# Kernel optimization log

Hardware: AMD Instinct MI355X
Metric: run time of the kernel (lower is better)

The kernel has to match this reference:

```python
import jax, jax.numpy as jnp
import numpy as np

S = 3000    # number of candidate spans (rows of g_i)
P = 80000   # total (mention, antecedent) pairs
GI = 768    # gi_dim
DD = 20     # distance/genre/speaker embedding dim
HID = 150   # mlp hidden dim (fixed in source)
ORDER = 2   # N: one higher-order refinement pass


def setup_inputs() -> dict:
    key = jax.random.key(0)
    ks = jax.random.split(key, 18)
    gij = 3 * GI + 3 * DD
    g_i = jax.random.normal(ks[0], (S, GI), jnp.float32)
    mention_scores = jax.random.normal(ks[1], (S, 1), jnp.float32)
    # sorted segment ids: ragged antecedent counts per mention, grouped contiguously
    mention_ids = jnp.sort(jax.random.randint(ks[2], (P,), 0, S, dtype=jnp.int32))
    antecedent_ids = jax.random.randint(ks[3], (P,), 0, S, dtype=jnp.int32)
    dist_bins = jax.random.randint(ks[4], (P,), 0, 10, dtype=jnp.int32)
    genre_ids = jax.random.randint(ks[5], (P,), 0, 7, dtype=jnp.int32) + 1   # 1..7, 0 is padding_idx
    speaker_ids = jax.random.randint(ks[6], (P,), 0, 2, dtype=jnp.int32) + 1  # 1..2, 0 is padding_idx
    w = lambda k, shp: 0.02 * jax.random.normal(k, shp, jnp.float32)
    dist_emb = w(ks[7], (10, DD))
    genre_emb = w(ks[8], (8, DD)).at[0].set(0.0)     # padding_idx=0
    speaker_emb = w(ks[9], (3, DD)).at[0].set(0.0)   # padding_idx=0
    W1 = w(ks[10], (gij, HID)); b1 = jnp.zeros((HID,), jnp.float32)
    W2 = w(ks[11], (HID, HID)); b2 = jnp.zeros((HID,), jnp.float32)
    W3 = w(ks[12], (HID, 1)); b3 = jnp.zeros((1,), jnp.float32)
    Wf = w(ks[13], (2 * GI, 1)); bf = jnp.zeros((1,), jnp.float32)
    return {"g_i": g_i, "mention_scores": mention_scores, "mention_ids": mention_ids,
            "antecedent_ids": antecedent_ids, "dist_bins": dist_bins, "genre_ids": genre_ids,
            "speaker_ids": speaker_ids, "dist_emb": dist_emb, "genre_emb": genre_emb,
            "speaker_emb": speaker_emb, "W1": W1, "b1": b1, "W2": W2, "b2": b2,
            "W3": W3, "b3": b3, "Wf": Wf, "bf": bf}


def _mlp(x, W1, b1, W2, b2, W3, b3):
    h = jax.nn.relu(x @ W1 + b1)
    h = jax.nn.relu(h @ W2 + b2)
    return h @ W3 + b3


def reference(g_i, mention_scores, mention_ids, antecedent_ids, dist_bins, genre_ids,
              speaker_ids, dist_emb, genre_emb, speaker_emb, W1, b1, W2, b2, W3, b3, Wf, bf):
    phi = jnp.concatenate([dist_emb[dist_bins], genre_emb[genre_ids], speaker_emb[speaker_ids]], axis=1)  # [P,60]
    seg = dict(num_segments=S, indices_are_sorted=True)
    g = g_i
    scores = None
    for n in range(ORDER):
        i_g = g[mention_ids]                # [P,GI] gather
        j_g = g[antecedent_ids]             # [P,GI] gather
        pairs = jnp.concatenate([i_g, j_g, i_g * j_g, phi], axis=1)  # [P,gij]
        scores = _mlp(pairs, W1, b1, W2, b2, W3, b3)                 # [P,1]
        if n < ORDER - 1:
            # higher_order_refinement: ragged segment softmax + weighted scatter update
            s = scores[:, 0]
            seg_max = jax.ops.segment_max(s, mention_ids, **seg)
            safe_max = jnp.where(jnp.isfinite(seg_max), seg_max, 0.0)
            e = jnp.exp(s - safe_max[mention_ids])
            denom = jax.ops.segment_sum(e, mention_ids, **seg)
            attn = e / jnp.where(denom > 0, denom, 1.0)[mention_ids]
            weighted = jax.ops.segment_sum(attn[:, None] * j_g, mention_ids, **seg)  # [S,GI]
            counts = jax.ops.segment_sum(jnp.ones_like(s), mention_ids, **seg)
            f = jax.nn.sigmoid(jnp.concatenate([g, weighted], axis=1) @ Wf + bf)  # [S,1]
            # NOTE: faithful to the source bug: f * mention_id (the integer index), not f * mention_g
            ids_f = jnp.arange(S, dtype=g.dtype)[:, None]
            g_new = f * ids_f + (1.0 - f) * weighted
            g = jnp.where(counts[:, None] > 0, g_new, g)
    s_i = mention_scores[mention_ids]
    s_j = mention_scores[antecedent_ids]
    coref_scores = s_i + s_j + scores       # [P,1]
    # segment softmax with an extra epsilon (score 0) logit per mention
    c = coref_scores[:, 0]
    seg_max = jax.ops.segment_max(c, mention_ids, **seg)
    m = jnp.maximum(jnp.where(jnp.isfinite(seg_max), seg_max, 0.0), 0.0)  # include epsilon logit 0
    e = jnp.exp(c - m[mention_ids])
    denom = jax.ops.segment_sum(e, mention_ids, **seg) + jnp.exp(-m)
    pair_probs = e / denom[mention_ids]     # [P]
    eps_probs = jnp.exp(-m) / denom         # [S]
    return coref_scores, pair_probs, eps_probs
```

## Files before the change

### kernel.cpp

```cpp
#include <hip/hip_runtime.h>

#define GI   768
#define HID  150
#define HPAD 160
#define DDIM 20

typedef __attribute__((ext_vector_type(8))) short v8s;
typedef __attribute__((ext_vector_type(4))) float f32x4;
typedef __attribute__((ext_vector_type(16))) float f32x16;

#define MFMA(A, B, C)   __builtin_amdgcn_mfma_f32_32x32x16_bf16(A, B, C, 0, 0, 0)
#define MFMA16(A, B, C) __builtin_amdgcn_mfma_f32_16x16x32_bf16(A, B, C, 0, 0, 0)

__device__ __forceinline__ ushort bf16rn(float x) {
  unsigned u = __float_as_uint(x);
  return (ushort)((u + 0x7fffu + ((u >> 16) & 1u)) >> 16);
}
__device__ __forceinline__ void bsplit(float x, ushort& h, ushort& l) {
  h = bf16rn(x);
  float fh = __uint_as_float((unsigned)h << 16);
  l = bf16rn(x - fh);
}
__device__ __forceinline__ void tsplit(float x, ushort& h, ushort& l) {
  unsigned u = __float_as_uint(x);
  h = (ushort)(u >> 16);
  float d = x - __uint_as_float(u & 0xffff0000u);
  l = (ushort)(__float_as_uint(d) >> 16);
}
__device__ __forceinline__ uint4 pack8(const ushort* v) {
  uint4 r;
  r.x = v[0] | ((unsigned)v[1] << 16); r.y = v[2] | ((unsigned)v[3] << 16);
  r.z = v[4] | ((unsigned)v[5] << 16); r.w = v[6] | ((unsigned)v[7] << 16);
  return r;
}
__device__ __forceinline__ v8s mk8(const ushort* v) {
  union { uint4 u; v8s s; } t;
  t.u = pack8(v);
  return t.s;
}

__device__ __forceinline__ void stage16(const ushort* gsrc, ushort* ldst) {
  __builtin_amdgcn_global_load_lds(
      (const __attribute__((address_space(1))) unsigned int*)(const void*)gsrc,
      (__attribute__((address_space(3))) unsigned int*)(void*)ldst, 16, 0, 0);
}

__global__ void seg_kernel(const int* __restrict__ mI, int* __restrict__ segs,
                           int P, int S) {
  int m = blockIdx.x * 256 + threadIdx.x;
  if (m > S) return;
  int lo = 0, hi = P;
  while (lo < hi) { int mid = (lo + hi) >> 1; if (mI[mid] < m) lo = mid + 1; else hi = mid; }
  segs[m] = lo;
}

__global__ void phi_kernel(const float* __restrict__ de, const float* __restrict__ ge,
                           const float* __restrict__ se, const float* __restrict__ W1,
                           float* __restrict__ phiW) {
  int idx = blockIdx.x * 256 + threadIdx.x;
  if (idx >= 21 * HPAD) return;
  int row = idx / HPAD, h = idx % HPAD;
  float v = 0.f;
  if (h < HID) {
    const float* emb; int off;
    if (row < 10)      { emb = de + row * DDIM;        off = 0; }
    else if (row < 18) { emb = ge + (row - 10) * DDIM; off = DDIM; }
    else               { emb = se + (row - 18) * DDIM; off = 2 * DDIM; }
    for (int k = 0; k < DDIM; ++k) v += emb[k] * W1[(3 * GI + off + k) * HID + h];
  }
  phiW[row * HPAD + h] = v;
}

#define NWS  (48 * 10 * 512)
#define NW16 (20 * 24 * 512)
#define NW2B (5 * 10 * 512)
__global__ void pad2_kernel(const float* __restrict__ W1, const float* __restrict__ W2,
                            const float* __restrict__ b1, const float* __restrict__ b2,
                            const float* __restrict__ W3,
                            ushort* __restrict__ WS,
                            ushort* __restrict__ W16hi, ushort* __restrict__ W16lo,
                            ushort* __restrict__ W2Bhi, ushort* __restrict__ W2Blo,
                            float* __restrict__ b1p, float2* __restrict__ b2w3) {
  int idx = blockIdx.x * 256 + threadIdx.x;
  if (idx < NWS) {
    int s = idx / (10 * 512); int r1 = idx % (10 * 512);
    int fi = r1 / 512; int r2 = r1 % 512;
    int l = r2 / 8, j = r2 % 8;
    int c = fi >> 1, hl = fi & 1;
    int h = c * 32 + (l & 31);
    int k = s * 16 + 8 * (l >> 5) + j;
    float x = (h < HID) ? W1[(size_t)(2 * GI + k) * HID + h] : 0.f;
    ushort hh, ll; bsplit(x, hh, ll);
    WS[idx] = hl ? ll : hh; return;
  }
  idx -= NWS;
  if (idx < NW16) {
    int ct = idx / (24 * 512); int r1 = idx % (24 * 512);
    int s = r1 / 512; int r2 = r1 % 512;
    int l = r2 / 8, j = r2 % 8;
    int col = ct * 16 + (l & 15);
    int k = s * 32 + 8 * (l >> 4) + j;
    int seg = col / HPAD, h = col % HPAD;
    float x = (h < HID) ? W1[(size_t)(seg * GI + k) * HID + h] : 0.f;
    ushort hh, ll; bsplit(x, hh, ll);
    W16hi[idx] = hh; W16lo[idx] = ll; return;
  }
  idx -= NW16;
  if (idx < NW2B) {
    int rt = idx / (10 * 512); int r1 = idx % (10 * 512);
    int s = r1 / 512; int r2 = r1 % 512;
    int l = r2 / 8, j = r2 % 8;
    int h2 = rt * 32 + (l & 31);
    int k = s * 16 + 8 * (l >> 5) + j;
    float x = (k < HID && h2 < HID) ? W2[(size_t)k * HID + h2] : 0.f;
    ushort hh, ll; bsplit(x, hh, ll);
    W2Bhi[idx] = hh; W2Blo[idx] = ll; return;
  }
  idx -= NW2B;
  if (idx < HPAD) { b1p[idx] = (idx < HID) ? b1[idx] : 0.f; return; }
  idx -= HPAD;
  if (idx < HPAD) {
    b2w3[idx] = make_float2((idx < HID) ? b2[idx] : 0.f, (idx < HID) ? W3[idx] : 0.f);
    return;
  }
}

__global__ __launch_bounds__(64, 4) void pre3_kernel(
    const float* __restrict__ g, const ushort* __restrict__ W16hi,
    const ushort* __restrict__ W16lo, float* __restrict__ pre, int S) {
  const int lane = threadIdx.x;
  const int ct = blockIdx.x;
  const int row0 = blockIdx.y * 16;
  int srow = row0 + (lane & 15); if (srow >= S) srow = S - 1;
  const float* gp = g + (size_t)srow * GI + 8 * (lane >> 4);
  const ushort* wph = W16hi + ((size_t)ct * 24 * 64 + lane) * 8;
  const ushort* wpl = W16lo + ((size_t)ct * 24 * 64 + lane) * 8;

  f32x4 acc = {};
#pragma unroll 2
  for (int s = 0; s < 24; ++s) {
    const float4 a0 = *(const float4*)(gp + s * 32);
    const float4 a1 = *(const float4*)(gp + s * 32 + 4);
    const v8s bh = *(const v8s*)(wph + (size_t)s * 512);
    const v8s bl = *(const v8s*)(wpl + (size_t)s * 512);
    float xr[8] = {a0.x, a0.y, a0.z, a0.w, a1.x, a1.y, a1.z, a1.w};
    ushort hs[8], ls[8];
#pragma unroll
    for (int j = 0; j < 8; ++j) tsplit(xr[j], hs[j], ls[j]);
    const v8s ah = mk8(hs), al = mk8(ls);
    acc = MFMA16(ah, bh, acc);
    acc = MFMA16(al, bh, acc);
    acc = MFMA16(ah, bl, acc);
  }
  const int col = ct * 16 + (lane & 15);
#pragma unroll
  for (int r = 0; r < 4; ++r) {
    int sr = row0 + (lane >> 4) * 4 + r;
    if (sr < S) pre[(size_t)sr * 320 + col] = acc[r];
  }
}

__global__ __launch_bounds__(256, 3) void h1b_kernel(
    const float* __restrict__ g, const float* __restrict__ pre,
    const float* __restrict__ phiW, const ushort* __restrict__ WS,
    const float* __restrict__ b1p,
    const int* __restrict__ mI, const int* __restrict__ aI,
    const int* __restrict__ db, const int* __restrict__ ge, const int* __restrict__ sp,
    ushort* __restrict__ h1hi, ushort* __restrict__ h1lo, int P) {
  __shared__ ushort wbuf[2][10 * 512];

  const int t = threadIdx.x;
  const int lane = t & 63, wv = t >> 6;
  const int lcol = lane & 31, half = lane >> 5;

  const int nwg = gridDim.x;
  const int orig = blockIdx.x;
  const int xcd = orig & 7, idx8 = orig >> 3;
  const int qq = nwg >> 3, rq = nwg & 7;
  const int wg = (xcd < rq ? xcd * (qq + 1) : rq * (qq + 1) + (xcd - rq) * qq) + idx8;
  const int p0w = wg * 128 + wv * 32;

  const int myp = p0w + lcol;
  const int iA = mI[myp], jA = aI[myp];
  const int rdL = db[myp], rgL = 10 + ge[myp], rsL = 18 + sp[myp];

  const float* gi = g + (size_t)iA * GI + 8 * half;
  const float* gj = g + (size_t)jA * GI + 8 * half;

  const int f0 = 2 * wv, f1 = 2 * wv + 1;
  const int f2 = (wv < 2) ? 8 + wv : -1;

  f32x16 acc[5];
  {
    f32x16 z = {};
#pragma unroll
    for (int c = 0; c < 5; ++c) acc[c] = z;
  }

  {
    const ushort* base = WS + (size_t)0 * 10 * 512;
    stage16(base + f0 * 512 + lane * 8, &wbuf[0][f0 * 512]);
    stage16(base + f1 * 512 + lane * 8, &wbuf[0][f1 * 512]);
    if (f2 >= 0) stage16(base + f2 * 512 + lane * 8, &wbuf[0][f2 * 512]);
  }
  asm volatile("s_waitcnt vmcnt(0)" ::: "memory");
  __syncthreads();

  int cur = 0;
#pragma unroll 2
  for (int s = 0; s < 48; ++s) {
    if (s + 1 < 48) {
      const ushort* base = WS + (size_t)(s + 1) * 10 * 512;
      ushort* dst = wbuf[cur ^ 1];
      stage16(base + f0 * 512 + lane * 8, dst + f0 * 512);
      stage16(base + f1 * 512 + lane * 8, dst + f1 * 512);
      if (f2 >= 0) stage16(base + f2 * 512 + lane * 8, dst + f2 * 512);
    }
    const int d0 = s * 16;
    const float4 a0 = *(const float4*)(gi + d0);
    const float4 a1 = *(const float4*)(gi + d0 + 4);
    const float4 b0 = *(const float4*)(gj + d0);
    const float4 b1v = *(const float4*)(gj + d0 + 4);
    float xr[8] = {a0.x * b0.x, a0.y * b0.y, a0.z * b0.z, a0.w * b0.w,
                   a1.x * b1v.x, a1.y * b1v.y, a1.z * b1v.z, a1.w * b1v.w};
    ushort hs[8], ls[8];
#pragma unroll
    for (int j = 0; j < 8; ++j) tsplit(xr[j], hs[j], ls[j]);
    const v8s ah = mk8(hs), al = mk8(ls);
    const ushort* wb = wbuf[cur];
#pragma unroll
    for (int c = 0; c < 5; ++c) {
      const v8s wh = *(const v8s*)(wb + (2 * c) * 512 + lane * 8);
      const v8s wl = *(const v8s*)(wb + (2 * c + 1) * 512 + lane * 8);
      acc[c] = MFMA(ah, wh, acc[c]);
      acc[c] = MFMA(al, wh, acc[c]);
      acc[c] = MFMA(ah, wl, acc[c]);
    }
    asm volatile("s_waitcnt vmcnt(0)" ::: "memory");
    __syncthreads();
    cur ^= 1;
  }

#pragma unroll
  for (int q = 0; q < 16; ++q) {
    const int rr2 = (q & 3) + 8 * (q >> 2) + 4 * half;
    const int pI = __shfl(iA, rr2);
    const int pJ = __shfl(jA, rr2);
    const int rd = __shfl(rdL, rr2), rg = __shfl(rgL, rr2), rs = __shfl(rsL, rr2);
    const float* preI = pre + (size_t)pI * 320;
    const float* preJ = pre + (size_t)pJ * 320 + 160;
    const size_t prow = (size_t)(p0w + rr2) * 160;
#pragma unroll
    for (int c = 0; c < 5; ++c) {
      const int col = c * 32 + lcol;
      float v = acc[c][q] + b1p[col] + preI[col] + preJ[col]
              + phiW[rd * HPAD + col] + phiW[rg * HPAD + col] + phiW[rs * HPAD + col];
      v = fmaxf(v, 0.f);
      ushort hh, ll; tsplit(v, hh, ll);
      h1hi[prow + col] = hh;
      h1lo[prow + col] = ll;
    }
  }
}

__global__ __launch_bounds__(64, 3) void score3_kernel(
    const ushort* __restrict__ h1hi, const ushort* __restrict__ h1lo,
    const ushort* __restrict__ W2Bhi, const ushort* __restrict__ W2Blo,
    const float2* __restrict__ b2w3, const float* __restrict__ b3,
    float* __restrict__ sOut, int P) {
  const int lane = threadIdx.x;
  const int lcol = lane & 31, half = lane >> 5;
  const int p0 = blockIdx.x * 32;

  const ushort* hh = h1hi + (size_t)(p0 + lcol) * 160 + 8 * half;
  const ushort* hl = h1lo + (size_t)(p0 + lcol) * 160 + 8 * half;

  f32x16 acc[5];
  {
    f32x16 z = {};
#pragma unroll
    for (int r = 0; r < 5; ++r) acc[r] = z;
  }

#pragma unroll 2
  for (int s = 0; s < 10; ++s) {
    const v8s bh = *(const v8s*)(hh + s * 16);
    const v8s bl = *(const v8s*)(hl + s * 16);
#pragma unroll
    for (int r = 0; r < 5; ++r) {
      const size_t o = ((size_t)(r * 10 + s) * 64 + lane) * 8;
      const v8s ah = *(const v8s*)(W2Bhi + o);
      const v8s al = *(const v8s*)(W2Blo + o);
      acc[r] = MFMA(ah, bh, acc[r]);
      acc[r] = MFMA(al, bh, acc[r]);
      acc[r] = MFMA(ah, bl, acc[r]);
    }
  }

  float part = 0.f;
#pragma unroll
  for (int r = 0; r < 5; ++r) {
#pragma unroll
    for (int q = 0; q < 16; ++q) {
      const int h2 = r * 32 + (q & 3) + 8 * (q >> 2) + 4 * half;
      const float2 bw = b2w3[h2];
      part += fmaxf(acc[r][q] + bw.x, 0.f) * bw.y;
    }
  }
  part += __shfl_xor(part, 32);
  if (lane < 32) sOut[p0 + lane] = part + b3[0];
}

__global__ void mid_kernel(const float* __restrict__ g, const float* __restrict__ s1,
                           const int* __restrict__ segs, const int* __restrict__ aI,
                           const float* __restrict__ Wf, const float* __restrict__ bf,
                           float* __restrict__ g2) {
  const int m = blockIdx.x;
  const int t = threadIdx.x;
  const int st = segs[m], en = segs[m + 1], n = en - st;
  if (n == 0) {
    for (int d = t; d < GI; d += 256) g2[m * GI + d] = g[m * GI + d];
    return;
  }
  __shared__ float red[256];
  __shared__ float wred[4][GI];
  float mx = -INFINITY;
  for (int p = st + t; p < en; p += 256) mx = fmaxf(mx, s1[p]);
  red[t] = mx; __syncthreads();
  for (int s = 128; s > 0; s >>= 1) { if (t < s) red[t] = fmaxf(red[t], red[t + s]); __syncthreads(); }
  mx = red[0]; __syncthreads();
  const int dg = t & 63, pg = t >> 6;
  float wv[12];
#pragma unroll
  for (int u = 0; u < 12; ++u) wv[u] = 0.f;
  float esum = 0.f;
  for (int p = st + pg; p < en; p += 4) {
    const float e = expf(s1[p] - mx);
    esum += e;
    const float* gj = g + (size_t)aI[p] * GI + dg;
#pragma unroll
    for (int u = 0; u < 12; ++u) wv[u] += e * gj[u * 64];
  }
  red[t] = (dg == 0) ? esum : 0.f; __syncthreads();
  for (int s = 128; s > 0; s >>= 1) { if (t < s) red[t] += red[t + s]; __syncthreads(); }
  const float denom = red[0]; __syncthreads();
#pragma unroll
  for (int u = 0; u < 12; ++u) wred[pg][dg + u * 64] = wv[u];
  __syncthreads();
  float part = 0.f;
  float wfin[3];
#pragma unroll
  for (int u = 0; u < 3; ++u) {
    const int d = t + u * 256;
    float ws = (wred[0][d] + wred[1][d] + wred[2][d] + wred[3][d]) / denom;
    wfin[u] = ws;
    part += g[(size_t)m * GI + d] * Wf[d] + ws * Wf[GI + d];
  }
  red[t] = part; __syncthreads();
  for (int s = 128; s > 0; s >>= 1) { if (t < s) red[t] += red[t + s]; __syncthreads(); }
  const float f = 1.f / (1.f + expf(-(red[0] + bf[0])));
#pragma unroll
  for (int u = 0; u < 3; ++u) {
    const int d = t + u * 256;
    g2[(size_t)m * GI + d] = f * (float)m + (1.f - f) * wfin[u];
  }
}

__global__ void coref_kernel(const float* __restrict__ ms, const float* __restrict__ s2,
                             const int* __restrict__ mI, const int* __restrict__ aI,
                             float* __restrict__ out, int P) {
  int p = blockIdx.x * 256 + threadIdx.x;
  if (p >= P) return;
  out[p] = ms[mI[p]] + ms[aI[p]] + s2[p];
}

__global__ void final_kernel(const float* __restrict__ c, const int* __restrict__ segs,
                             float* __restrict__ pairP, float* __restrict__ epsP) {
  const int m = blockIdx.x;
  const int t = threadIdx.x;
  const int st = segs[m], en = segs[m + 1], n = en - st;
  __shared__ float red[256];
  float mx = -INFINITY;
  for (int p = st + t; p < en; p += 256) mx = fmaxf(mx, c[p]);
  red[t] = mx; __syncthreads();
  for (int s = 128; s > 0; s >>= 1) { if (t < s) red[t] = fmaxf(red[t], red[t + s]); __syncthreads(); }
  mx = red[0]; __syncthreads();
  const float m2 = (n > 0) ? fmaxf(mx, 0.f) : 0.f;
  float sm = 0.f;
  for (int p = st + t; p < en; p += 256) sm += expf(c[p] - m2);
  red[t] = sm; __syncthreads();
  for (int s = 128; s > 0; s >>= 1) { if (t < s) red[t] += red[t + s]; __syncthreads(); }
  const float denom = red[0] + expf(-m2);
  for (int p = st + t; p < en; p += 256) pairP[p] = expf(c[p] - m2) / denom;
  if (t == 0) epsP[m] = expf(-m2) / denom;
}

extern "C" void kernel_launch(void* const* d_in, const int* in_sizes, int n_in,
                              void* d_out, int out_size, void* d_ws, size_t ws_size,
                              hipStream_t stream) {
  const float* g_i  = (const float*)d_in[0];
  const float* ms   = (const float*)d_in[1];
  const int*   mI   = (const int*)d_in[2];
  const int*   aI   = (const int*)d_in[3];
  const int*   db   = (const int*)d_in[4];
  const int*   ge   = (const int*)d_in[5];
  const int*   sp   = (const int*)d_in[6];
  const float* de   = (const float*)d_in[7];
  const float* gemb = (const float*)d_in[8];
  const float* semb = (const float*)d_in[9];
  const float* W1   = (const float*)d_in[10];
  const float* b1   = (const float*)d_in[11];
  const float* W2   = (const float*)d_in[12];
  const float* b2   = (const float*)d_in[13];
  const float* W3   = (const float*)d_in[14];
  const float* b3   = (const float*)d_in[15];
  const float* Wf   = (const float*)d_in[16];
  const float* bf   = (const float*)d_in[17];

  const int S = in_sizes[0] / GI;
  const int P = in_sizes[2];
  float* out = (float*)d_out;

  char* ws = (char*)d_ws;
  size_t off = 0;
  auto take = [&](size_t bytes) -> char* {
    char* p = ws + off;
    off = (off + bytes + 15) & ~(size_t)15;
    return p;
  };
  int*    segs  = (int*)   take((size_t)(S + 1) * 4);
  float*  phiW  = (float*) take((size_t)21 * HPAD * 4);
  float*  pre   = (float*) take((size_t)S * 320 * 4);
  float*  g2    = (float*) take((size_t)S * GI * 4);
  float*  s1    = (float*) take((size_t)P * 4);
  float*  s2    = (float*) take((size_t)P * 4);
  ushort* WS    = (ushort*)take((size_t)NWS * 2);
  ushort* W16hi = (ushort*)take((size_t)NW16 * 2);
  ushort* W16lo = (ushort*)take((size_t)NW16 * 2);
  ushort* W2Bhi = (ushort*)take((size_t)NW2B * 2);
  ushort* W2Blo = (ushort*)take((size_t)NW2B * 2);
  float*  b1p   = (float*) take((size_t)HPAD * 4);
  float2* b2w3  = (float2*)take((size_t)HPAD * 8);
  ushort* h1hi  = (ushort*)take((size_t)P * 160 * 2);
  ushort* h1lo  = (ushort*)take((size_t)P * 160 * 2);

  const int gridSeg = (S + 1 + 255) / 256;
  const int gridPhi = (21 * HPAD + 255) / 256;
  const int padTot  = NWS + NW16 + NW2B + 2 * HPAD;
  const int gridPad = (padTot + 255) / 256;
  const dim3 gridPre(20, (S + 15) / 16);
  const int gridH   = P / 128;
  const int gridS3  = P / 32;
  const int gridCor = (P + 255) / 256;

  seg_kernel<<<gridSeg, 256, 0, stream>>>(mI, segs, P, S);
  phi_kernel<<<gridPhi, 256, 0, stream>>>(de, gemb, semb, W1, phiW);
  pad2_kernel<<<gridPad, 256, 0, stream>>>(W1, W2, b1, b2, W3, WS,
                                           W16hi, W16lo, W2Bhi, W2Blo, b1p, b2w3);

  pre3_kernel<<<gridPre, 64, 0, stream>>>(g_i, W16hi, W16lo, pre, S);
  h1b_kernel<<<gridH, 256, 0, stream>>>(g_i, pre, phiW, WS, b1p,
                                        mI, aI, db, ge, sp, h1hi, h1lo, P);
  score3_kernel<<<gridS3, 64, 0, stream>>>(h1hi, h1lo, W2Bhi, W2Blo, b2w3, b3, s1, P);
  mid_kernel<<<S, 256, 0, stream>>>(g_i, s1, segs, aI, Wf, bf, g2);

  pre3_kernel<<<gridPre, 64, 0, stream>>>(g2, W16hi, W16lo, pre, S);
  h1b_kernel<<<gridH, 256, 0, stream>>>(g2, pre, phiW, WS, b1p,
                                        mI, aI, db, ge, sp, h1hi, h1lo, P);
  score3_kernel<<<gridS3, 64, 0, stream>>>(h1hi, h1lo, W2Bhi, W2Blo, b2w3, b3, s2, P);

  coref_kernel<<<gridCor, 256, 0, stream>>>(ms, s2, mI, aI, out, P);
  final_kernel<<<S, 256, 0, stream>>>(out, segs, out + P, out + 2 * (size_t)P);
}
```

Before: 472.3 us.

## Drop low-order weight and activation splits, single-wave h1 kernel without LDS staging

Weights W1 (both the pair-product part and the per-span part) are now stored as a single bf16 copy instead of a hi/lo split, so the pre and h1 kernels issue two MFMAs per step instead of three. The h1 activations are stored as one bf16 value rather than a hi/lo pair, which halves h1 memory traffic and drops a third MFMA in score3. The h1 kernel moves from 256-thread blocks with double-buffered LDS weight staging to 64-thread blocks that read weights straight from global memory, which removes barriers but gives up sharing the staged weights within a block. Accuracy goes down because the weights and h1 keep fewer mantissa bits, and this may break the tolerance.

```diff
diff --git a/kernel.cpp b/kernel.cpp
--- a/kernel.cpp
+++ b/kernel.cpp
@@ -15,11 +15,6 @@
 __device__ __forceinline__ ushort bf16rn(float x) {
   unsigned u = __float_as_uint(x);
   return (ushort)((u + 0x7fffu + ((u >> 16) & 1u)) >> 16);
-}
-__device__ __forceinline__ void bsplit(float x, ushort& h, ushort& l) {
-  h = bf16rn(x);
-  float fh = __uint_as_float((unsigned)h << 16);
-  l = bf16rn(x - fh);
 }
 __device__ __forceinline__ void tsplit(float x, ushort& h, ushort& l) {
   unsigned u = __float_as_uint(x);
@@ -37,12 +32,6 @@
   union { uint4 u; v8s s; } t;
   t.u = pack8(v);
   return t.s;
-}
-
-__device__ __forceinline__ void stage16(const ushort* gsrc, ushort* ldst) {
-  __builtin_amdgcn_global_load_lds(
-      (const __attribute__((address_space(1))) unsigned int*)(const void*)gsrc,
-      (__attribute__((address_space(3))) unsigned int*)(void*)ldst, 16, 0, 0);
 }
 
 __global__ void seg_kernel(const int* __restrict__ mI, int* __restrict__ segs,
@@ -71,29 +60,26 @@
   phiW[row * HPAD + h] = v;
 }
 
-#define NWS  (48 * 10 * 512)
+#define NWH  (48 * 5 * 512)
 #define NW16 (20 * 24 * 512)
 #define NW2B (5 * 10 * 512)
 __global__ void pad2_kernel(const float* __restrict__ W1, const float* __restrict__ W2,
                             const float* __restrict__ b1, const float* __restrict__ b2,
                             const float* __restrict__ W3,
-                            ushort* __restrict__ WS,
-                            ushort* __restrict__ W16hi, ushort* __restrict__ W16lo,
+                            ushort* __restrict__ WH, ushort* __restrict__ W16,
                             ushort* __restrict__ W2Bhi, ushort* __restrict__ W2Blo,
                             float* __restrict__ b1p, float2* __restrict__ b2w3) {
   int idx = blockIdx.x * 256 + threadIdx.x;
-  if (idx < NWS) {
-    int s = idx / (10 * 512); int r1 = idx % (10 * 512);
-    int fi = r1 / 512; int r2 = r1 % 512;
+  if (idx < NWH) {
+    int s = idx / (5 * 512); int r1 = idx % (5 * 512);
+    int c = r1 / 512; int r2 = r1 % 512;
     int l = r2 / 8, j = r2 % 8;
-    int c = fi >> 1, hl = fi & 1;
     int h = c * 32 + (l & 31);
     int k = s * 16 + 8 * (l >> 5) + j;
     float x = (h < HID) ? W1[(size_t)(2 * GI + k) * HID + h] : 0.f;
-    ushort hh, ll; bsplit(x, hh, ll);
-    WS[idx] = hl ? ll : hh; return;
-  }
-  idx -= NWS;
+    WH[idx] = bf16rn(x); return;
+  }
+  idx -= NWH;
   if (idx < NW16) {
     int ct = idx / (24 * 512); int r1 = idx % (24 * 512);
     int s = r1 / 512; int r2 = r1 % 512;
@@ -102,8 +88,7 @@
     int k = s * 32 + 8 * (l >> 4) + j;
     int seg = col / HPAD, h = col % HPAD;
     float x = (h < HID) ? W1[(size_t)(seg * GI + k) * HID + h] : 0.f;
-    ushort hh, ll; bsplit(x, hh, ll);
-    W16hi[idx] = hh; W16lo[idx] = ll; return;
+    W16[idx] = bf16rn(x); return;
   }
   idx -= NW16;
   if (idx < NW2B) {
@@ -113,8 +98,9 @@
     int h2 = rt * 32 + (l & 31);
     int k = s * 16 + 8 * (l >> 5) + j;
     float x = (k < HID && h2 < HID) ? W2[(size_t)k * HID + h2] : 0.f;
-    ushort hh, ll; bsplit(x, hh, ll);
-    W2Bhi[idx] = hh; W2Blo[idx] = ll; return;
+    ushort hh = bf16rn(x);
+    float lo = x - __uint_as_float((unsigned)hh << 16);
+    W2Bhi[idx] = hh; W2Blo[idx] = bf16rn(lo); return;
   }
   idx -= NW2B;
   if (idx < HPAD) { b1p[idx] = (idx < HID) ? b1[idx] : 0.f; return; }
@@ -126,23 +112,21 @@
 }
 
 __global__ __launch_bounds__(64, 4) void pre3_kernel(
-    const float* __restrict__ g, const ushort* __restrict__ W16hi,
-    const ushort* __restrict__ W16lo, float* __restrict__ pre, int S) {
+    const float* __restrict__ g, const ushort* __restrict__ W16,
+    float* __restrict__ pre, int S) {
   const int lane = threadIdx.x;
   const int ct = blockIdx.x;
   const int row0 = blockIdx.y * 16;
   int srow = row0 + (lane & 15); if (srow >= S) srow = S - 1;
   const float* gp = g + (size_t)srow * GI + 8 * (lane >> 4);
-  const ushort* wph = W16hi + ((size_t)ct * 24 * 64 + lane) * 8;
-  const ushort* wpl = W16lo + ((size_t)ct * 24 * 64 + lane) * 8;
+  const ushort* wp = W16 + ((size_t)ct * 24 * 64 + lane) * 8;
 
   f32x4 acc = {};
 #pragma unroll 2
   for (int s = 0; s < 24; ++s) {
     const float4 a0 = *(const float4*)(gp + s * 32);
     const float4 a1 = *(const float4*)(gp + s * 32 + 4);
-    const v8s bh = *(const v8s*)(wph + (size_t)s * 512);
-    const v8s bl = *(const v8s*)(wpl + (size_t)s * 512);
+    const v8s bh = *(const v8s*)(wp + (size_t)s * 512);
     float xr[8] = {a0.x, a0.y, a0.z, a0.w, a1.x, a1.y, a1.z, a1.w};
     ushort hs[8], ls[8];
 #pragma unroll
@@ -150,7 +134,6 @@
     const v8s ah = mk8(hs), al = mk8(ls);
     acc = MFMA16(ah, bh, acc);
     acc = MFMA16(al, bh, acc);
-    acc = MFMA16(ah, bl, acc);
   }
   const int col = ct * 16 + (lane & 15);
 #pragma unroll
@@ -160,17 +143,14 @@
   }
 }
 
-__global__ __launch_bounds__(256, 3) void h1b_kernel(
+__global__ __launch_bounds__(64, 3) void h1a_kernel(
     const float* __restrict__ g, const float* __restrict__ pre,
-    const float* __restrict__ phiW, const ushort* __restrict__ WS,
+    const float* __restrict__ phiW, const ushort* __restrict__ WH,
     const float* __restrict__ b1p,
     const int* __restrict__ mI, const int* __restrict__ aI,
     const int* __restrict__ db, const int* __restrict__ ge, const int* __restrict__ sp,
-    ushort* __restrict__ h1hi, ushort* __restrict__ h1lo, int P) {
-  __shared__ ushort wbuf[2][10 * 512];
-
-  const int t = threadIdx.x;
-  const int lane = t & 63, wv = t >> 6;
+    ushort* __restrict__ h1b, int P) {
+  const int lane = threadIdx.x;
   const int lcol = lane & 31, half = lane >> 5;
 
   const int nwg = gridDim.x;
@@ -178,17 +158,14 @@
   const int xcd = orig & 7, idx8 = orig >> 3;
   const int qq = nwg >> 3, rq = nwg & 7;
   const int wg = (xcd < rq ? xcd * (qq + 1) : rq * (qq + 1) + (xcd - rq) * qq) + idx8;
-  const int p0w = wg * 128 + wv * 32;
-
-  const int myp = p0w + lcol;
+  const int p0 = wg * 32;
+
+  const int myp = p0 + lcol;
   const int iA = mI[myp], jA = aI[myp];
   const int rdL = db[myp], rgL = 10 + ge[myp], rsL = 18 + sp[myp];
 
   const float* gi = g + (size_t)iA * GI + 8 * half;
   const float* gj = g + (size_t)jA * GI + 8 * half;
-
-  const int f0 = 2 * wv, f1 = 2 * wv + 1;
-  const int f2 = (wv < 2) ? 8 + wv : -1;
 
   f32x16 acc[5];
   {
@@ -197,25 +174,8 @@
     for (int c = 0; c < 5; ++c) acc[c] = z;
   }
 
-  {
-    const ushort* base = WS + (size_t)0 * 10 * 512;
-    stage16(base + f0 * 512 + lane * 8, &wbuf[0][f0 * 512]);
-    stage16(base + f1 * 512 + lane * 8, &wbuf[0][f1 * 512]);
-    if (f2 >= 0) stage16(base + f2 * 512 + lane * 8, &wbuf[0][f2 * 512]);
-  }
-  asm volatile("s_waitcnt vmcnt(0)" ::: "memory");
-  __syncthreads();
-
-  int cur = 0;
 #pragma unroll 2
   for (int s = 0; s < 48; ++s) {
-    if (s + 1 < 48) {
-      const ushort* base = WS + (size_t)(s + 1) * 10 * 512;
-      ushort* dst = wbuf[cur ^ 1];
-      stage16(base + f0 * 512 + lane * 8, dst + f0 * 512);
-      stage16(base + f1 * 512 + lane * 8, dst + f1 * 512);
-      if (f2 >= 0) stage16(base + f2 * 512 + lane * 8, dst + f2 * 512);
-    }
     const int d0 = s * 16;
     const float4 a0 = *(const float4*)(gi + d0);
     const float4 a1 = *(const float4*)(gi + d0 + 4);
@@ -227,18 +187,13 @@
 #pragma unroll
     for (int j = 0; j < 8; ++j) tsplit(xr[j], hs[j], ls[j]);
     const v8s ah = mk8(hs), al = mk8(ls);
-    const ushort* wb = wbuf[cur];
 #pragma unroll
     for (int c = 0; c < 5; ++c) {
-      const v8s wh = *(const v8s*)(wb + (2 * c) * 512 + lane * 8);
-      const v8s wl = *(const v8s*)(wb + (2 * c + 1) * 512 + lane * 8);
+      const size_t o = (((size_t)s * 5 + c) * 64 + lane) * 8;
+      const v8s wh = *(const v8s*)(WH + o);
       acc[c] = MFMA(ah, wh, acc[c]);
       acc[c] = MFMA(al, wh, acc[c]);
-      acc[c] = MFMA(ah, wl, acc[c]);
     }
-    asm volatile("s_waitcnt vmcnt(0)" ::: "memory");
-    __syncthreads();
-    cur ^= 1;
   }
 
 #pragma unroll
@@ -249,22 +204,20 @@
     const int rd = __shfl(rdL, rr2), rg = __shfl(rgL, rr2), rs = __shfl(rsL, rr2);
     const float* preI = pre + (size_t)pI * 320;
     const float* preJ = pre + (size_t)pJ * 320 + 160;
-    const size_t prow = (size_t)(p0w + rr2) * 160;
+    const size_t prow = (size_t)(p0 + rr2) * 160;
 #pragma unroll
     for (int c = 0; c < 5; ++c) {
       const int col = c * 32 + lcol;
       float v = acc[c][q] + b1p[col] + preI[col] + preJ[col]
               + phiW[rd * HPAD + col] + phiW[rg * HPAD + col] + phiW[rs * HPAD + col];
       v = fmaxf(v, 0.f);
-      ushort hh, ll; tsplit(v, hh, ll);
-      h1hi[prow + col] = hh;
-      h1lo[prow + col] = ll;
+      h1b[prow + col] = bf16rn(v);
     }
   }
 }
 
 __global__ __launch_bounds__(64, 3) void score3_kernel(
-    const ushort* __restrict__ h1hi, const ushort* __restrict__ h1lo,
+    const ushort* __restrict__ h1b,
     const ushort* __restrict__ W2Bhi, const ushort* __restrict__ W2Blo,
     const float2* __restrict__ b2w3, const float* __restrict__ b3,
     float* __restrict__ sOut, int P) {
@@ -272,8 +225,7 @@
   const int lcol = lane & 31, half = lane >> 5;
   const int p0 = blockIdx.x * 32;
 
-  const ushort* hh = h1hi + (size_t)(p0 + lcol) * 160 + 8 * half;
-  const ushort* hl = h1lo + (size_t)(p0 + lcol) * 160 + 8 * half;
+  const ushort* hb = h1b + (size_t)(p0 + lcol) * 160 + 8 * half;
 
   f32x16 acc[5];
   {
@@ -284,16 +236,14 @@
 
 #pragma unroll 2
   for (int s = 0; s < 10; ++s) {
-    const v8s bh = *(const v8s*)(hh + s * 16);
-    const v8s bl = *(const v8s*)(hl + s * 16);
+    const v8s b = *(const v8s*)(hb + s * 16);
 #pragma unroll
     for (int r = 0; r < 5; ++r) {
       const size_t o = ((size_t)(r * 10 + s) * 64 + lane) * 8;
       const v8s ah = *(const v8s*)(W2Bhi + o);
       const v8s al = *(const v8s*)(W2Blo + o);
-      acc[r] = MFMA(ah, bh, acc[r]);
-      acc[r] = MFMA(al, bh, acc[r]);
-      acc[r] = MFMA(ah, bl, acc[r]);
+      acc[r] = MFMA(ah, b, acc[r]);
+      acc[r] = MFMA(al, b, acc[r]);
     }
   }
 
@@ -352,9 +302,9 @@
 #pragma unroll
   for (int u = 0; u < 3; ++u) {
     const int d = t + u * 256;
-    float ws = (wred[0][d] + wred[1][d] + wred[2][d] + wred[3][d]) / denom;
-    wfin[u] = ws;
-    part += g[(size_t)m * GI + d] * Wf[d] + ws * Wf[GI + d];
+    float wsv = (wred[0][d] + wred[1][d] + wred[2][d] + wred[3][d]) / denom;
+    wfin[u] = wsv;
+    part += g[(size_t)m * GI + d] * Wf[d] + wsv * Wf[GI + d];
   }
   red[t] = part; __syncthreads();
   for (int s = 128; s > 0; s >>= 1) { if (t < s) red[t] += red[t + s]; __syncthreads(); }
@@ -434,40 +384,37 @@
   float*  g2    = (float*) take((size_t)S * GI * 4);
   float*  s1    = (float*) take((size_t)P * 4);
   float*  s2    = (float*) take((size_t)P * 4);
-  ushort* WS    = (ushort*)take((size_t)NWS * 2);
-  ushort* W16hi = (ushort*)take((size_t)NW16 * 2);
-  ushort* W16lo = (ushort*)take((size_t)NW16 * 2);
+  ushort* WH    = (ushort*)take((size_t)NWH * 2);
+  ushort* W16   = (ushort*)take((size_t)NW16 * 2);
   ushort* W2Bhi = (ushort*)take((size_t)NW2B * 2);
   ushort* W2Blo = (ushort*)take((size_t)NW2B * 2);
   float*  b1p   = (float*) take((size_t)HPAD * 4);
   float2* b2w3  = (float2*)take((size_t)HPAD * 8);
-  ushort* h1hi  = (ushort*)take((size_t)P * 160 * 2);
-  ushort* h1lo  = (ushort*)take((size_t)P * 160 * 2);
+  ushort* h1b   = (ushort*)take((size_t)P * 160 * 2);
 
   const int gridSeg = (S + 1 + 255) / 256;
   const int gridPhi = (21 * HPAD + 255) / 256;
-  const int padTot  = NWS + NW16 + NW2B + 2 * HPAD;
+  const int padTot  = NWH + NW16 + NW2B + 2 * HPAD;
   const int gridPad = (padTot + 255) / 256;
   const dim3 gridPre(20, (S + 15) / 16);
-  const int gridH   = P / 128;
-  const int gridS3  = P / 32;
+  const int gridH   = P / 32;
   const int gridCor = (P + 255) / 256;
 
   seg_kernel<<<gridSeg, 256, 0, stream>>>(mI, segs, P, S);
   phi_kernel<<<gridPhi, 256, 0, stream>>>(de, gemb, semb, W1, phiW);
-  pad2_kernel<<<gridPad, 256, 0, stream>>>(W1, W2, b1, b2, W3, WS,
-                                           W16hi, W16lo, W2Bhi, W2Blo, b1p, b2w3);
-
-  pre3_kernel<<<gridPre, 64, 0, stream>>>(g_i, W16hi, W16lo, pre, S);
-  h1b_kernel<<<gridH, 256, 0, stream>>>(g_i, pre, phiW, WS, b1p,
-                                        mI, aI, db, ge, sp, h1hi, h1lo, P);
-  score3_kernel<<<gridS3, 64, 0, stream>>>(h1hi, h1lo, W2Bhi, W2Blo, b2w3, b3, s1, P);
+  pad2_kernel<<<gridPad, 256, 0, stream>>>(W1, W2, b1, b2, W3, WH, W16,
+                                           W2Bhi, W2Blo, b1p, b2w3);
+
+  pre3_kernel<<<gridPre, 64, 0, stream>>>(g_i, W16, pre, S);
+  h1a_kernel<<<gridH, 64, 0, stream>>>(g_i, pre, phiW, WH, b1p,
+                                       mI, aI, db, ge, sp, h1b, P);
+  score3_kernel<<<gridH, 64, 0, stream>>>(h1b, W2Bhi, W2Blo, b2w3, b3, s1, P);
   mid_kernel<<<S, 256, 0, stream>>>(g_i, s1, segs, aI, Wf, bf, g2);
 
-  pre3_kernel<<<gridPre, 64, 0, stream>>>(g2, W16hi, W16lo, pre, S);
-  h1b_kernel<<<gridH, 256, 0, stream>>>(g2, pre, phiW, WS, b1p,
-                                        mI, aI, db, ge, sp, h1hi, h1lo, P);
-  score3_kernel<<<gridS3, 64, 0, stream>>>(h1hi, h1lo, W2Bhi, W2Blo, b2w3, b3, s2, P);
+  pre3_kernel<<<gridPre, 64, 0, stream>>>(g2, W16, pre, S);
+  h1a_kernel<<<gridH, 64, 0, stream>>>(g2, pre, phiW, WH, b1p,
+                                       mI, aI, db, ge, sp, h1b, P);
+  score3_kernel<<<gridH, 64, 0, stream>>>(h1b, W2Bhi, W2Blo, b2w3, b3, s2, P);
 
   coref_kernel<<<gridCor, 256, 0, stream>>>(ms, s2, mI, aI, out, P);
   final_kernel<<<S, 256, 0, stream>>>(out, segs, out + P, out + 2 * (size_t)P);
```

Measured after the change: 473.2 us. Within noise of the previous version (+0.2%).
